# Kernel tuning notes

Measured on AMD Instinct MI355X. Metric: run time of the kernel, lower is better.

The kernel has to match this reference:

```python
import jax, jax.numpy as jnp
import numpy as np

HEAD_DIM = 64
SCALE = 1.0 / np.sqrt(HEAD_DIM)  # canonical 1/sqrt(d_k)


def setup_inputs() -> dict:
    key = jax.random.key(0)
    kq, kk, kv = jax.random.split(key, 3)
    B, Lq, Lk, D = 16, 2048, 2048, HEAD_DIM
    q = jax.random.normal(kq, (B, Lq, D), dtype=jnp.float32)
    k = jax.random.normal(kk, (B, Lk, D), dtype=jnp.float32)
    v = jax.random.normal(kv, (B, Lk, D), dtype=jnp.float32)
    return {"q": q, "k": k, "v": v}


def reference(q, k, v):
    # scores: [B, Lq, Lk] = q @ k^T, scaled by 1/sqrt(d)
    scores = jnp.einsum("bqd,bkd->bqk", q, k) * SCALE
    # softmax over the key axis (dim=2), numerically stable
    attention = jax.nn.softmax(scores, axis=2)
    # dropout prob = 0.0 -> identity
    context = jnp.einsum("bqk,bkd->bqd", attention, v)  # [B, Lq, D]
    return (context, attention)
```

## Files before the change

### kernel.cpp

```cpp
#include <hip/hip_runtime.h>
#include <hip/hip_bf16.h>

#define B_   16
#define LQ   2048
#define LK   2048
#define HD   64
#define QT   32
#define KT   64
#define NKT  (LK / KT)
#define NWG  (B_ * (LQ / QT))
#define NXCD 8
#define EC   0.1803368801f

typedef __attribute__((ext_vector_type(8))) short bf16x8;
typedef __attribute__((ext_vector_type(4))) float f32x4;

#define MFMA __builtin_amdgcn_mfma_f32_16x16x32_bf16

__device__ __forceinline__ int swz(int row, int col) {
    return (row << 6) + (col ^ ((row & 7) << 3));
}

__device__ __forceinline__ bf16x8 cvt8(float4 a, float4 b) {
    union { bf16x8 v; __hip_bfloat162 h[4]; } u;
    u.h[0] = __float22bfloat162_rn(make_float2(a.x, a.y));
    u.h[1] = __float22bfloat162_rn(make_float2(a.z, a.w));
    u.h[2] = __float22bfloat162_rn(make_float2(b.x, b.y));
    u.h[3] = __float22bfloat162_rn(make_float2(b.z, b.w));
    return u.v;
}
__device__ __forceinline__ bf16x8 cvt8s(const float* v) {
    union { bf16x8 r; __hip_bfloat162 h[4]; } u;
    #pragma unroll
    for (int i = 0; i < 4; ++i)
        u.h[i] = __float22bfloat162_rn(make_float2(v[2 * i], v[2 * i + 1]));
    return u.r;
}
__device__ __forceinline__ unsigned short bfbits(float x) {
    union { __hip_bfloat16 h; unsigned short s; } u;
    u.h = __float2bfloat16(x);
    return u.s;
}

__global__ __launch_bounds__(256, 4) void sdpa_kernel(
    const float* __restrict__ qg, const float* __restrict__ kg,
    const float* __restrict__ vg, float* __restrict__ ctx,
    float* __restrict__ att)
{
    __shared__ unsigned short Pb[2][QT * KT];
    __shared__ float redl[4][QT];
    __shared__ float invl[QT];

    const int tid  = threadIdx.x;
    const int wave = tid >> 6;
    const int lane = tid & 63;
    const int g    = lane >> 4;
    const int c    = lane & 15;

    const int bid = (int)blockIdx.x;
    const int lid = (bid % NXCD) * (NWG / NXCD) + bid / NXCD;

    const int b  = lid / (LQ / QT);
    const int qt = lid % (LQ / QT);

    const float* qp = qg + (size_t)(b * LQ + qt * QT) * HD;
    const float* kp = kg + (size_t)b * LK * HD;
    const float* vp = vg + (size_t)b * LK * HD;
    float* ctxp = ctx + (size_t)(b * LQ + qt * QT) * HD;
    float* attp = att + (size_t)(b * LQ + qt * QT) * LK;

    bf16x8 aQ[2][2];
    #pragma unroll
    for (int m = 0; m < 2; ++m)
        #pragma unroll
        for (int h = 0; h < 2; ++h) {
            const float* p = qp + (m * 16 + c) * HD + h * 32 + g * 8;
            aQ[m][h] = cvt8(*reinterpret_cast<const float4*>(p),
                            *reinterpret_cast<const float4*>(p + 4));
        }

    const float* kl = kp + (wave * 16 + c) * HD + g * 8;
    const float* vl = vp + (g * 8) * HD + wave * 16 + c;

    float lsum[2][4] = {{0.f,0.f,0.f,0.f},{0.f,0.f,0.f,0.f}};
    float4 ka0 = *reinterpret_cast<const float4*>(kl);
    float4 ka1 = *reinterpret_cast<const float4*>(kl + 4);
    float4 kb0 = *reinterpret_cast<const float4*>(kl + 32);
    float4 kb1 = *reinterpret_cast<const float4*>(kl + 36);
    #pragma unroll 1
    for (int t = 0; t < NKT; ++t) {
        bf16x8 bK0 = cvt8(ka0, ka1);
        bf16x8 bK1 = cvt8(kb0, kb1);
        if (t + 1 < NKT) {
            const float* n = kl + (size_t)(t + 1) * KT * HD;
            ka0 = *reinterpret_cast<const float4*>(n);
            ka1 = *reinterpret_cast<const float4*>(n + 4);
            kb0 = *reinterpret_cast<const float4*>(n + 32);
            kb1 = *reinterpret_cast<const float4*>(n + 36);
        }
        #pragma unroll
        for (int m = 0; m < 2; ++m) {
            f32x4 acc = {0.f, 0.f, 0.f, 0.f};
            acc = MFMA(aQ[m][0], bK0, acc, 0, 0, 0);
            acc = MFMA(aQ[m][1], bK1, acc, 0, 0, 0);
            #pragma unroll
            for (int r = 0; r < 4; ++r)
                lsum[m][r] += exp2f(acc[r] * EC);
        }
    }

    #pragma unroll
    for (int m = 0; m < 2; ++m)
        #pragma unroll
        for (int r = 0; r < 4; ++r) {
            float s = lsum[m][r];
            s += __shfl_xor(s, 1, 64);
            s += __shfl_xor(s, 2, 64);
            s += __shfl_xor(s, 4, 64);
            s += __shfl_xor(s, 8, 64);
            lsum[m][r] = s;
        }
    if (c == 0) {
        #pragma unroll
        for (int m = 0; m < 2; ++m)
            #pragma unroll
            for (int r = 0; r < 4; ++r)
                redl[wave][m * 16 + g * 4 + r] = lsum[m][r];
    }
    __syncthreads();
    if (tid < QT) {
        float s = redl[0][tid] + redl[1][tid] + redl[2][tid] + redl[3][tid];
        invl[tid] = 1.0f / s;
    }
    __syncthreads();

    float il[2][4];
    #pragma unroll
    for (int m = 0; m < 2; ++m)
        #pragma unroll
        for (int r = 0; r < 4; ++r)
            il[m][r] = invl[m * 16 + g * 4 + r];

    f32x4 cacc[2];
    cacc[0] = (f32x4){0.f, 0.f, 0.f, 0.f};
    cacc[1] = (f32x4){0.f, 0.f, 0.f, 0.f};

    ka0 = *reinterpret_cast<const float4*>(kl);
    ka1 = *reinterpret_cast<const float4*>(kl + 4);
    kb0 = *reinterpret_cast<const float4*>(kl + 32);
    kb1 = *reinterpret_cast<const float4*>(kl + 36);
    float va[8], vb[8];
    #pragma unroll
    for (int j = 0; j < 8; ++j) {
        va[j] = vl[(size_t)j * HD];
        vb[j] = vl[(size_t)(32 + j) * HD];
    }

    int buf = 0;
    #pragma unroll 1
    for (int t = 0; t < NKT; ++t) {
        bf16x8 bK0 = cvt8(ka0, ka1);
        bf16x8 bK1 = cvt8(kb0, kb1);
        bf16x8 bV0 = cvt8s(va);
        bf16x8 bV1 = cvt8s(vb);

        float pr[2][4];
        #pragma unroll
        for (int m = 0; m < 2; ++m) {
            f32x4 acc = {0.f, 0.f, 0.f, 0.f};
            acc = MFMA(aQ[m][0], bK0, acc, 0, 0, 0);
            acc = MFMA(aQ[m][1], bK1, acc, 0, 0, 0);
            #pragma unroll
            for (int r = 0; r < 4; ++r)
                pr[m][r] = exp2f(acc[r] * EC) * il[m][r];
        }

        if (t + 1 < NKT) {
            const float* n = kl + (size_t)(t + 1) * KT * HD;
            ka0 = *reinterpret_cast<const float4*>(n);
            ka1 = *reinterpret_cast<const float4*>(n + 4);
            kb0 = *reinterpret_cast<const float4*>(n + 32);
            kb1 = *reinterpret_cast<const float4*>(n + 36);
            const float* nv = vl + (size_t)(t + 1) * KT * HD;
            #pragma unroll
            for (int j = 0; j < 8; ++j) {
                va[j] = nv[(size_t)j * HD];
                vb[j] = nv[(size_t)(32 + j) * HD];
            }
        }

        #pragma unroll
        for (int m = 0; m < 2; ++m)
            #pragma unroll
            for (int r = 0; r < 4; ++r) {
                int row = m * 16 + g * 4 + r;
                int col = wave * 16 + c;
                attp[(size_t)row * LK + t * KT + col] = pr[m][r];
                Pb[buf][swz(row, col)] = bfbits(pr[m][r]);
            }

        asm volatile("s_waitcnt lgkmcnt(0)\n\ts_barrier" ::: "memory");

        #pragma unroll
        for (int m = 0; m < 2; ++m) {
            bf16x8 aP0 = *reinterpret_cast<const bf16x8*>(&Pb[buf][swz(m * 16 + c, g * 8)]);
            bf16x8 aP1 = *reinterpret_cast<const bf16x8*>(&Pb[buf][swz(m * 16 + c, 32 + g * 8)]);
            cacc[m] = MFMA(aP0, bV0, cacc[m], 0, 0, 0);
            cacc[m] = MFMA(aP1, bV1, cacc[m], 0, 0, 0);
        }
        buf ^= 1;
    }

    #pragma unroll
    for (int m = 0; m < 2; ++m)
        #pragma unroll
        for (int r = 0; r < 4; ++r)
            ctxp[(m * 16 + g * 4 + r) * HD + wave * 16 + c] = cacc[m][r];
}

extern "C" void kernel_launch(void* const* d_in, const int* in_sizes, int n_in,
                              void* d_out, int out_size, void* d_ws, size_t ws_size,
                              hipStream_t stream) {
    const float* q = (const float*)d_in[0];
    const float* k = (const float*)d_in[1];
    const float* v = (const float*)d_in[2];
    float* ctx = (float*)d_out;
    float* att = ctx + (size_t)B_ * LQ * HD;
    dim3 grid(NWG);
    sdpa_kernel<<<grid, dim3(256), 0, stream>>>(q, k, v, ctx, att);
}
```

Baseline: 207.7 us.

## Stage probabilities across four key tiles and write attention with vector nontemporal stores

Groups four key tiles per outer step, staging bf16 probabilities for all of them in a wider shared buffer. After the PV MFMAs, each wave reads rows back from shared memory and writes the attention matrix as 16-byte nontemporal float4 stores instead of scattered scalar stores. This targets the cost of the uncoalesced writes of the large attention output and halves barrier frequency. In exchange, attention values are now rounded through bf16, which reduces output precision and may affect tolerance.

After: 265.7 us. +27.9%, slower.

```diff
diff --git a/kernel.cpp b/kernel.cpp
--- a/kernel.cpp
+++ b/kernel.cpp
@@ -7,18 +7,22 @@
 #define HD   64
 #define QT   32
 #define KT   64
+#define STT  4
+#define SKT  (KT * STT)
 #define NKT  (LK / KT)
+#define NST  (LK / SKT)
 #define NWG  (B_ * (LQ / QT))
 #define NXCD 8
 #define EC   0.1803368801f
 
 typedef __attribute__((ext_vector_type(8))) short bf16x8;
 typedef __attribute__((ext_vector_type(4))) float f32x4;
+typedef __attribute__((ext_vector_type(4))) unsigned short us4;
 
 #define MFMA __builtin_amdgcn_mfma_f32_16x16x32_bf16
 
-__device__ __forceinline__ int swz(int row, int col) {
-    return (row << 6) + (col ^ ((row & 7) << 3));
+__device__ __forceinline__ int pidx(int row, int sub, int col) {
+    return row * SKT + sub * KT + (col ^ ((row & 7) << 3));
 }
 
 __device__ __forceinline__ bf16x8 cvt8(float4 a, float4 b) {
@@ -41,13 +45,17 @@
     u.h = __float2bfloat16(x);
     return u.s;
 }
+__device__ __forceinline__ float bf2f(unsigned short s) {
+    union { unsigned u; float f; } v; v.u = ((unsigned)s) << 16;
+    return v.f;
+}
 
 __global__ __launch_bounds__(256, 4) void sdpa_kernel(
     const float* __restrict__ qg, const float* __restrict__ kg,
     const float* __restrict__ vg, float* __restrict__ ctx,
     float* __restrict__ att)
 {
-    __shared__ unsigned short Pb[2][QT * KT];
+    __shared__ unsigned short PbF[QT * SKT];
     __shared__ float redl[4][QT];
     __shared__ float invl[QT];
 
@@ -149,66 +157,85 @@
     ka1 = *reinterpret_cast<const float4*>(kl + 4);
     kb0 = *reinterpret_cast<const float4*>(kl + 32);
     kb1 = *reinterpret_cast<const float4*>(kl + 36);
-    float va[8], vb[8];
+    float vt[16];
     #pragma unroll
     for (int j = 0; j < 8; ++j) {
-        va[j] = vl[(size_t)j * HD];
-        vb[j] = vl[(size_t)(32 + j) * HD];
-    }
-
-    int buf = 0;
+        vt[j]     = vl[(size_t)j * HD];
+        vt[8 + j] = vl[(size_t)(32 + j) * HD];
+    }
+
+    const int so_c4  = lane * 4;
+    const int so_sub = so_c4 >> 6;
+    const int so_cc  = so_c4 & 63;
+
     #pragma unroll 1
-    for (int t = 0; t < NKT; ++t) {
-        bf16x8 bK0 = cvt8(ka0, ka1);
-        bf16x8 bK1 = cvt8(kb0, kb1);
-        bf16x8 bV0 = cvt8s(va);
-        bf16x8 bV1 = cvt8s(vb);
-
-        float pr[2][4];
-        #pragma unroll
-        for (int m = 0; m < 2; ++m) {
-            f32x4 acc = {0.f, 0.f, 0.f, 0.f};
-            acc = MFMA(aQ[m][0], bK0, acc, 0, 0, 0);
-            acc = MFMA(aQ[m][1], bK1, acc, 0, 0, 0);
-            #pragma unroll
-            for (int r = 0; r < 4; ++r)
-                pr[m][r] = exp2f(acc[r] * EC) * il[m][r];
-        }
-
-        if (t + 1 < NKT) {
-            const float* n = kl + (size_t)(t + 1) * KT * HD;
-            ka0 = *reinterpret_cast<const float4*>(n);
-            ka1 = *reinterpret_cast<const float4*>(n + 4);
-            kb0 = *reinterpret_cast<const float4*>(n + 32);
-            kb1 = *reinterpret_cast<const float4*>(n + 36);
-            const float* nv = vl + (size_t)(t + 1) * KT * HD;
-            #pragma unroll
-            for (int j = 0; j < 8; ++j) {
-                va[j] = nv[(size_t)j * HD];
-                vb[j] = nv[(size_t)(32 + j) * HD];
+    for (int st = 0; st < NST; ++st) {
+        bf16x8 bV[STT][2];
+        #pragma unroll
+        for (int sub = 0; sub < STT; ++sub) {
+            const int t = st * STT + sub;
+            bf16x8 bK0 = cvt8(ka0, ka1);
+            bf16x8 bK1 = cvt8(kb0, kb1);
+            bV[sub][0] = cvt8s(vt);
+            bV[sub][1] = cvt8s(vt + 8);
+            if (t + 1 < NKT) {
+                const float* n = kl + (size_t)(t + 1) * KT * HD;
+                ka0 = *reinterpret_cast<const float4*>(n);
+                ka1 = *reinterpret_cast<const float4*>(n + 4);
+                kb0 = *reinterpret_cast<const float4*>(n + 32);
+                kb1 = *reinterpret_cast<const float4*>(n + 36);
+                const float* nv = vl + (size_t)(t + 1) * KT * HD;
+                #pragma unroll
+                for (int j = 0; j < 8; ++j) {
+                    vt[j]     = nv[(size_t)j * HD];
+                    vt[8 + j] = nv[(size_t)(32 + j) * HD];
+                }
             }
-        }
-
-        #pragma unroll
-        for (int m = 0; m < 2; ++m)
-            #pragma unroll
-            for (int r = 0; r < 4; ++r) {
-                int row = m * 16 + g * 4 + r;
-                int col = wave * 16 + c;
-                attp[(size_t)row * LK + t * KT + col] = pr[m][r];
-                Pb[buf][swz(row, col)] = bfbits(pr[m][r]);
+            float pr[2][4];
+            #pragma unroll
+            for (int m = 0; m < 2; ++m) {
+                f32x4 acc = {0.f, 0.f, 0.f, 0.f};
+                acc = MFMA(aQ[m][0], bK0, acc, 0, 0, 0);
+                acc = MFMA(aQ[m][1], bK1, acc, 0, 0, 0);
+                #pragma unroll
+                for (int r = 0; r < 4; ++r)
+                    pr[m][r] = exp2f(acc[r] * EC) * il[m][r];
             }
+            #pragma unroll
+            for (int m = 0; m < 2; ++m)
+                #pragma unroll
+                for (int r = 0; r < 4; ++r)
+                    PbF[pidx(m * 16 + g * 4 + r, sub, wave * 16 + c)] =
+                        bfbits(pr[m][r]);
+        }
 
         asm volatile("s_waitcnt lgkmcnt(0)\n\ts_barrier" ::: "memory");
 
         #pragma unroll
-        for (int m = 0; m < 2; ++m) {
-            bf16x8 aP0 = *reinterpret_cast<const bf16x8*>(&Pb[buf][swz(m * 16 + c, g * 8)]);
-            bf16x8 aP1 = *reinterpret_cast<const bf16x8*>(&Pb[buf][swz(m * 16 + c, 32 + g * 8)]);
-            cacc[m] = MFMA(aP0, bV0, cacc[m], 0, 0, 0);
-            cacc[m] = MFMA(aP1, bV1, cacc[m], 0, 0, 0);
-        }
-        buf ^= 1;
+        for (int sub = 0; sub < STT; ++sub)
+            #pragma unroll
+            for (int m = 0; m < 2; ++m) {
+                bf16x8 aP0 = *reinterpret_cast<const bf16x8*>(
+                    &PbF[pidx(m * 16 + c, sub, g * 8)]);
+                bf16x8 aP1 = *reinterpret_cast<const bf16x8*>(
+                    &PbF[pidx(m * 16 + c, sub, 32 + g * 8)]);
+                cacc[m] = MFMA(aP0, bV[sub][0], cacc[m], 0, 0, 0);
+                cacc[m] = MFMA(aP1, bV[sub][1], cacc[m], 0, 0, 0);
+            }
+
+        #pragma unroll
+        for (int it = 0; it < 8; ++it) {
+            const int row = it * 4 + wave;
+            us4 p4 = *reinterpret_cast<const us4*>(&PbF[pidx(row, so_sub, so_cc)]);
+            f32x4 o;
+            o.x = bf2f(p4.x); o.y = bf2f(p4.y);
+            o.z = bf2f(p4.z); o.w = bf2f(p4.w);
+            f32x4* dst = reinterpret_cast<f32x4*>(
+                attp + (size_t)row * LK + st * SKT + so_c4);
+            __builtin_nontemporal_store(o, dst);
+        }
+
+        asm volatile("s_waitcnt lgkmcnt(0)\n\ts_barrier" ::: "memory");
     }
 
     #pragma unroll
```

## Add dedicated store waves writing attention via coalesced float4 from LDS

Applied to the files above, without the earlier changes.

Adds two extra waves per block that read the fp32 probability tile from shared memory and write the attention matrix with row-contiguous float4 stores. The compute waves no longer issue scattered scalar global stores, and the P tile is kept in fp32 with a new XOR swizzle and converted to bf16 at read time. This aims to cut store transaction overhead and overlap output writes with compute. The cost is doubled LDS for P, idle waves during the first pass, and a larger block that may reduce occupancy.

Measured after the change: 579.8 us. +179.2%, slower.

```diff
diff --git a/kernel.cpp b/kernel.cpp
--- a/kernel.cpp
+++ b/kernel.cpp
@@ -17,8 +17,8 @@
 
 #define MFMA __builtin_amdgcn_mfma_f32_16x16x32_bf16
 
-__device__ __forceinline__ int swz(int row, int col) {
-    return (row << 6) + (col ^ ((row & 7) << 3));
+__device__ __forceinline__ int idx32(int row, int col) {
+    return row * 64 + ((((col >> 2) ^ (row & 15)) << 2) | (col & 3));
 }
 
 __device__ __forceinline__ bf16x8 cvt8(float4 a, float4 b) {
@@ -36,18 +36,13 @@
         u.h[i] = __float22bfloat162_rn(make_float2(v[2 * i], v[2 * i + 1]));
     return u.r;
 }
-__device__ __forceinline__ unsigned short bfbits(float x) {
-    union { __hip_bfloat16 h; unsigned short s; } u;
-    u.h = __float2bfloat16(x);
-    return u.s;
-}
-
-__global__ __launch_bounds__(256, 4) void sdpa_kernel(
+
+__global__ __launch_bounds__(384, 6) void sdpa_kernel(
     const float* __restrict__ qg, const float* __restrict__ kg,
     const float* __restrict__ vg, float* __restrict__ ctx,
     float* __restrict__ att)
 {
-    __shared__ unsigned short Pb[2][QT * KT];
+    __shared__ float P32[2][QT * 64];
     __shared__ float redl[4][QT];
     __shared__ float invl[QT];
 
@@ -59,7 +54,6 @@
 
     const int bid = (int)blockIdx.x;
     const int lid = (bid % NXCD) * (NWG / NXCD) + bid / NXCD;
-
     const int b  = lid / (LQ / QT);
     const int qt = lid % (LQ / QT);
 
@@ -69,63 +63,67 @@
     float* ctxp = ctx + (size_t)(b * LQ + qt * QT) * HD;
     float* attp = att + (size_t)(b * LQ + qt * QT) * LK;
 
+    const int cw4 = wave & 3;
+    const float* kl = kp + (cw4 * 16 + c) * HD + g * 8;
+    const float* vl = vp + (g * 8) * HD + cw4 * 16 + c;
+
     bf16x8 aQ[2][2];
-    #pragma unroll
-    for (int m = 0; m < 2; ++m)
-        #pragma unroll
-        for (int h = 0; h < 2; ++h) {
-            const float* p = qp + (m * 16 + c) * HD + h * 32 + g * 8;
-            aQ[m][h] = cvt8(*reinterpret_cast<const float4*>(p),
-                            *reinterpret_cast<const float4*>(p + 4));
-        }
-
-    const float* kl = kp + (wave * 16 + c) * HD + g * 8;
-    const float* vl = vp + (g * 8) * HD + wave * 16 + c;
-
-    float lsum[2][4] = {{0.f,0.f,0.f,0.f},{0.f,0.f,0.f,0.f}};
-    float4 ka0 = *reinterpret_cast<const float4*>(kl);
-    float4 ka1 = *reinterpret_cast<const float4*>(kl + 4);
-    float4 kb0 = *reinterpret_cast<const float4*>(kl + 32);
-    float4 kb1 = *reinterpret_cast<const float4*>(kl + 36);
-    #pragma unroll 1
-    for (int t = 0; t < NKT; ++t) {
-        bf16x8 bK0 = cvt8(ka0, ka1);
-        bf16x8 bK1 = cvt8(kb0, kb1);
-        if (t + 1 < NKT) {
-            const float* n = kl + (size_t)(t + 1) * KT * HD;
-            ka0 = *reinterpret_cast<const float4*>(n);
-            ka1 = *reinterpret_cast<const float4*>(n + 4);
-            kb0 = *reinterpret_cast<const float4*>(n + 32);
-            kb1 = *reinterpret_cast<const float4*>(n + 36);
-        }
-        #pragma unroll
-        for (int m = 0; m < 2; ++m) {
-            f32x4 acc = {0.f, 0.f, 0.f, 0.f};
-            acc = MFMA(aQ[m][0], bK0, acc, 0, 0, 0);
-            acc = MFMA(aQ[m][1], bK1, acc, 0, 0, 0);
-            #pragma unroll
-            for (int r = 0; r < 4; ++r)
-                lsum[m][r] += exp2f(acc[r] * EC);
-        }
-    }
-
-    #pragma unroll
-    for (int m = 0; m < 2; ++m)
-        #pragma unroll
-        for (int r = 0; r < 4; ++r) {
-            float s = lsum[m][r];
-            s += __shfl_xor(s, 1, 64);
-            s += __shfl_xor(s, 2, 64);
-            s += __shfl_xor(s, 4, 64);
-            s += __shfl_xor(s, 8, 64);
-            lsum[m][r] = s;
-        }
-    if (c == 0) {
-        #pragma unroll
-        for (int m = 0; m < 2; ++m)
-            #pragma unroll
-            for (int r = 0; r < 4; ++r)
-                redl[wave][m * 16 + g * 4 + r] = lsum[m][r];
+    float il[2][4];
+
+    if (wave < 4) {
+        #pragma unroll
+        for (int m = 0; m < 2; ++m)
+            #pragma unroll
+            for (int h = 0; h < 2; ++h) {
+                const float* p = qp + (m * 16 + c) * HD + h * 32 + g * 8;
+                aQ[m][h] = cvt8(*reinterpret_cast<const float4*>(p),
+                                *reinterpret_cast<const float4*>(p + 4));
+            }
+
+        float lsum[2][4] = {{0.f,0.f,0.f,0.f},{0.f,0.f,0.f,0.f}};
+        float4 ka0 = *reinterpret_cast<const float4*>(kl);
+        float4 ka1 = *reinterpret_cast<const float4*>(kl + 4);
+        float4 kb0 = *reinterpret_cast<const float4*>(kl + 32);
+        float4 kb1 = *reinterpret_cast<const float4*>(kl + 36);
+        #pragma unroll 1
+        for (int t = 0; t < NKT; ++t) {
+            bf16x8 bK0 = cvt8(ka0, ka1);
+            bf16x8 bK1 = cvt8(kb0, kb1);
+            if (t + 1 < NKT) {
+                const float* n = kl + (size_t)(t + 1) * KT * HD;
+                ka0 = *reinterpret_cast<const float4*>(n);
+                ka1 = *reinterpret_cast<const float4*>(n + 4);
+                kb0 = *reinterpret_cast<const float4*>(n + 32);
+                kb1 = *reinterpret_cast<const float4*>(n + 36);
+            }
+            #pragma unroll
+            for (int m = 0; m < 2; ++m) {
+                f32x4 acc = {0.f, 0.f, 0.f, 0.f};
+                acc = MFMA(aQ[m][0], bK0, acc, 0, 0, 0);
+                acc = MFMA(aQ[m][1], bK1, acc, 0, 0, 0);
+                #pragma unroll
+                for (int r = 0; r < 4; ++r)
+                    lsum[m][r] += exp2f(acc[r] * EC);
+            }
+        }
+        #pragma unroll
+        for (int m = 0; m < 2; ++m)
+            #pragma unroll
+            for (int r = 0; r < 4; ++r) {
+                float s = lsum[m][r];
+                s += __shfl_xor(s, 1, 64);
+                s += __shfl_xor(s, 2, 64);
+                s += __shfl_xor(s, 4, 64);
+                s += __shfl_xor(s, 8, 64);
+                lsum[m][r] = s;
+            }
+        if (c == 0) {
+            #pragma unroll
+            for (int m = 0; m < 2; ++m)
+                #pragma unroll
+                for (int r = 0; r < 4; ++r)
+                    redl[wave][m * 16 + g * 4 + r] = lsum[m][r];
+        }
     }
     __syncthreads();
     if (tid < QT) {
@@ -133,89 +131,111 @@
         invl[tid] = 1.0f / s;
     }
     __syncthreads();
-
-    float il[2][4];
-    #pragma unroll
-    for (int m = 0; m < 2; ++m)
-        #pragma unroll
-        for (int r = 0; r < 4; ++r)
-            il[m][r] = invl[m * 16 + g * 4 + r];
+    if (wave < 4) {
+        #pragma unroll
+        for (int m = 0; m < 2; ++m)
+            #pragma unroll
+            for (int r = 0; r < 4; ++r)
+                il[m][r] = invl[m * 16 + g * 4 + r];
+    }
 
     f32x4 cacc[2];
     cacc[0] = (f32x4){0.f, 0.f, 0.f, 0.f};
     cacc[1] = (f32x4){0.f, 0.f, 0.f, 0.f};
 
-    ka0 = *reinterpret_cast<const float4*>(kl);
-    ka1 = *reinterpret_cast<const float4*>(kl + 4);
-    kb0 = *reinterpret_cast<const float4*>(kl + 32);
-    kb1 = *reinterpret_cast<const float4*>(kl + 36);
+    float4 ka0, ka1, kb0, kb1;
     float va[8], vb[8];
-    #pragma unroll
-    for (int j = 0; j < 8; ++j) {
-        va[j] = vl[(size_t)j * HD];
-        vb[j] = vl[(size_t)(32 + j) * HD];
+    if (wave < 4) {
+        ka0 = *reinterpret_cast<const float4*>(kl);
+        ka1 = *reinterpret_cast<const float4*>(kl + 4);
+        kb0 = *reinterpret_cast<const float4*>(kl + 32);
+        kb1 = *reinterpret_cast<const float4*>(kl + 36);
+        #pragma unroll
+        for (int j = 0; j < 8; ++j) {
+            va[j] = vl[(size_t)j * HD];
+            vb[j] = vl[(size_t)(32 + j) * HD];
+        }
     }
 
     int buf = 0;
     #pragma unroll 1
     for (int t = 0; t < NKT; ++t) {
-        bf16x8 bK0 = cvt8(ka0, ka1);
-        bf16x8 bK1 = cvt8(kb0, kb1);
-        bf16x8 bV0 = cvt8s(va);
-        bf16x8 bV1 = cvt8s(vb);
-
-        float pr[2][4];
-        #pragma unroll
-        for (int m = 0; m < 2; ++m) {
-            f32x4 acc = {0.f, 0.f, 0.f, 0.f};
-            acc = MFMA(aQ[m][0], bK0, acc, 0, 0, 0);
-            acc = MFMA(aQ[m][1], bK1, acc, 0, 0, 0);
+        bf16x8 bV0, bV1;
+        if (wave < 4) {
+            bf16x8 bK0 = cvt8(ka0, ka1);
+            bf16x8 bK1 = cvt8(kb0, kb1);
+            bV0 = cvt8s(va);
+            bV1 = cvt8s(vb);
+
+            float pr[2][4];
+            #pragma unroll
+            for (int m = 0; m < 2; ++m) {
+                f32x4 acc = {0.f, 0.f, 0.f, 0.f};
+                acc = MFMA(aQ[m][0], bK0, acc, 0, 0, 0);
+                acc = MFMA(aQ[m][1], bK1, acc, 0, 0, 0);
+                #pragma unroll
+                for (int r = 0; r < 4; ++r)
+                    pr[m][r] = exp2f(acc[r] * EC) * il[m][r];
+            }
+
+            if (t + 1 < NKT) {
+                const float* n = kl + (size_t)(t + 1) * KT * HD;
+                ka0 = *reinterpret_cast<const float4*>(n);
+                ka1 = *reinterpret_cast<const float4*>(n + 4);
+                kb0 = *reinterpret_cast<const float4*>(n + 32);
+                kb1 = *reinterpret_cast<const float4*>(n + 36);
+                const float* nv = vl + (size_t)(t + 1) * KT * HD;
+                #pragma unroll
+                for (int j = 0; j < 8; ++j) {
+                    va[j] = nv[(size_t)j * HD];
+                    vb[j] = nv[(size_t)(32 + j) * HD];
+                }
+            }
+
+            #pragma unroll
+            for (int m = 0; m < 2; ++m)
+                #pragma unroll
+                for (int r = 0; r < 4; ++r)
+                    P32[buf][idx32(m * 16 + g * 4 + r, wave * 16 + c)] = pr[m][r];
+        }
+
+        asm volatile("s_waitcnt lgkmcnt(0)\n\ts_barrier" ::: "memory");
+
+        if (wave < 4) {
+            #pragma unroll
+            for (int m = 0; m < 2; ++m) {
+                const int row = m * 16 + c;
+                float4 p0 = *reinterpret_cast<const float4*>(&P32[buf][idx32(row, g * 8)]);
+                float4 p1 = *reinterpret_cast<const float4*>(&P32[buf][idx32(row, g * 8 + 4)]);
+                float4 p2 = *reinterpret_cast<const float4*>(&P32[buf][idx32(row, 32 + g * 8)]);
+                float4 p3 = *reinterpret_cast<const float4*>(&P32[buf][idx32(row, 36 + g * 8)]);
+                bf16x8 aP0 = cvt8(p0, p1);
+                bf16x8 aP1 = cvt8(p2, p3);
+                cacc[m] = MFMA(aP0, bV0, cacc[m], 0, 0, 0);
+                cacc[m] = MFMA(aP1, bV1, cacc[m], 0, 0, 0);
+            }
+        } else {
+            const int sw  = wave - 4;
+            const int cwd = c * 4;
+            #pragma unroll
+            for (int i = 0; i < 4; ++i) {
+                const int row = sw * 16 + i * 4 + g;
+                float4 vdat = *reinterpret_cast<const float4*>(
+                    &P32[buf][idx32(row, cwd)]);
+                *reinterpret_cast<float4*>(
+                    attp + (size_t)row * LK + t * KT + cwd) = vdat;
+            }
+        }
+        buf ^= 1;
+    }
+
+    if (wave < 4) {
+        #pragma unroll
+        for (int m = 0; m < 2; ++m)
             #pragma unroll
             for (int r = 0; r < 4; ++r)
-                pr[m][r] = exp2f(acc[r] * EC) * il[m][r];
-        }
-
-        if (t + 1 < NKT) {
-            const float* n = kl + (size_t)(t + 1) * KT * HD;
-            ka0 = *reinterpret_cast<const float4*>(n);
-            ka1 = *reinterpret_cast<const float4*>(n + 4);
-            kb0 = *reinterpret_cast<const float4*>(n + 32);
-            kb1 = *reinterpret_cast<const float4*>(n + 36);
-            const float* nv = vl + (size_t)(t + 1) * KT * HD;
-            #pragma unroll
-            for (int j = 0; j < 8; ++j) {
-                va[j] = nv[(size_t)j * HD];
-                vb[j] = nv[(size_t)(32 + j) * HD];
-            }
-        }
-
-        #pragma unroll
-        for (int m = 0; m < 2; ++m)
-            #pragma unroll
-            for (int r = 0; r < 4; ++r) {
-                int row = m * 16 + g * 4 + r;
-                int col = wave * 16 + c;
-                attp[(size_t)row * LK + t * KT + col] = pr[m][r];
-                Pb[buf][swz(row, col)] = bfbits(pr[m][r]);
-            }
-
-        asm volatile("s_waitcnt lgkmcnt(0)\n\ts_barrier" ::: "memory");
-
-        #pragma unroll
-        for (int m = 0; m < 2; ++m) {
-            bf16x8 aP0 = *reinterpret_cast<const bf16x8*>(&Pb[buf][swz(m * 16 + c, g * 8)]);
-            bf16x8 aP1 = *reinterpret_cast<const bf16x8*>(&Pb[buf][swz(m * 16 + c, 32 + g * 8)]);
-            cacc[m] = MFMA(aP0, bV0, cacc[m], 0, 0, 0);
-            cacc[m] = MFMA(aP1, bV1, cacc[m], 0, 0, 0);
-        }
-        buf ^= 1;
-    }
-
-    #pragma unroll
-    for (int m = 0; m < 2; ++m)
-        #pragma unroll
-        for (int r = 0; r < 4; ++r)
-            ctxp[(m * 16 + g * 4 + r) * HD + wave * 16 + c] = cacc[m][r];
+                ctxp[(m * 16 + g * 4 + r) * HD + wave * 16 + c] = cacc[m][r];
+    }
 }
 
 extern "C" void kernel_launch(void* const* d_in, const int* in_sizes, int n_in,
@@ -227,5 +247,5 @@
     float* ctx = (float*)d_out;
     float* att = ctx + (size_t)B_ * LQ * HD;
     dim3 grid(NWG);
-    sdpa_kernel<<<grid, dim3(256), 0, stream>>>(q, k, v, ctx, att);
-}
+    sdpa_kernel<<<grid, dim3(384), 0, stream>>>(q, k, v, ctx, att);
+}
```
